# Optimization experiments

Measured on AMD Instinct MI355X. Metric: run time of the kernel, lower is better.

Reference implementation:

```python
import jax, jax.numpy as jnp
import numpy as np
from functools import partial

N_QUBITS = 8
DEPTH = 2
INPUT_DIM = 128
HIDDEN_DIM = N_QUBITS  # required: hx = o * tanh(cx) elementwise
DIM = 2 ** N_QUBITS

# Z expectation matrix: ZMAT[k, i] = +1/-1 depending on bit of basis state k at wire i
# (wire 0 is the most-significant qubit, PennyLane convention)
_bits = ((np.arange(DIM)[:, None] >> (N_QUBITS - 1 - np.arange(N_QUBITS)[None, :])) & 1)
ZMAT = jnp.asarray(1.0 - 2.0 * _bits, dtype=jnp.float32)  # [2**n, n]


def _apply_1q(state, G, wire):
    """Apply 2x2 gate G ([2,2] shared or [B,2,2] batched) on `wire`."""
    B = state.shape[0]
    left, right = 2 ** wire, 2 ** (N_QUBITS - wire - 1)
    s = state.reshape(B, left, 2, right)
    if G.ndim == 2:
        s = jnp.einsum('ij,bljr->blir', G, s)
    else:
        s = jnp.einsum('bij,bljr->blir', G, s)
    return s.reshape(B, DIM)


def _apply_cnot(state, wire):
    """CNOT with control=wire, target=wire+1 (adjacent)."""
    B = state.shape[0]
    left, right = 2 ** wire, 2 ** (N_QUBITS - wire - 2)
    s = state.reshape(B, left, 2, 2, right)
    s = jnp.concatenate([s[:, :, :1], s[:, :, 1:, ::-1]], axis=2)
    return s.reshape(B, DIM)


def quantum_gate(angles, params):
    """angles: [B, n] RX rotation angles; params: [depth, n] RY angles.
    Returns [B, n] PauliZ expectations (exact statevector simulation)."""
    B = angles.shape[0]
    state = jnp.zeros((B, DIM), dtype=jnp.complex64).at[:, 0].set(1.0)
    # RX encoding layer (batched angles)
    c = jnp.cos(angles / 2).astype(jnp.complex64)
    s = (-1j) * jnp.sin(angles / 2).astype(jnp.complex64)
    for i in range(N_QUBITS):
        G = jnp.stack([jnp.stack([c[:, i], s[:, i]], -1),
                       jnp.stack([s[:, i], c[:, i]], -1)], -2)  # [B,2,2]
        state = _apply_1q(state, G, i)
    # variational layers: RY (shared params) + CNOT chain
    cp = jnp.cos(params / 2).astype(jnp.complex64)
    sp = jnp.sin(params / 2).astype(jnp.complex64)
    for d in range(DEPTH):
        for i in range(N_QUBITS):
            G = jnp.array([[1.0, 0.0], [0.0, 1.0]], jnp.complex64)
            G = jnp.stack([jnp.stack([cp[d, i], -sp[d, i]]),
                           jnp.stack([sp[d, i], cp[d, i]])])  # [2,2]
            state = _apply_1q(state, G, i)
        for i in range(N_QUBITS - 1):
            state = _apply_cnot(state, i)
    probs = (state.real ** 2 + state.imag ** 2)  # [B, 2**n]
    return probs @ ZMAT  # [B, n]


def setup_inputs() -> dict:
    key = jax.random.key(0)
    ks = jax.random.split(key, 13)
    T, B = 256, 1024
    cat = INPUT_DIM + HIDDEN_DIM
    lin_scale = 1.0 / np.sqrt(cat)
    d = {'inputs': jax.random.normal(ks[0], (T, B, INPUT_DIM), jnp.float32)}
    for idx, g in enumerate(['f', 'i', 'g', 'o']):
        d[f'W{g}'] = jax.random.uniform(ks[1 + 3 * idx], (N_QUBITS, cat), jnp.float32, -lin_scale, lin_scale)
        d[f'b{g}'] = jax.random.uniform(ks[2 + 3 * idx], (N_QUBITS,), jnp.float32, -lin_scale, lin_scale)
        d[f'P{g}'] = jax.random.normal(ks[3 + 3 * idx], (DEPTH, N_QUBITS), jnp.float32)
    return d


def reference(inputs, Wf, bf, Pf, Wi, bi, Pi, Wg, bg, Pg, Wo, bo, Po):
    T, B, _ = inputs.shape
    h0 = jnp.zeros((B, HIDDEN_DIM), inputs.dtype)
    c0 = jnp.zeros((B, HIDDEN_DIM), inputs.dtype)

    def step(carry, x):
        hx, cx = carry
        comb = jnp.concatenate([x, hx], axis=1)  # [B, input+hidden]
        f = jax.nn.sigmoid(quantum_gate(comb @ Wf.T + bf, Pf))
        i = jax.nn.sigmoid(quantum_gate(comb @ Wi.T + bi, Pi))
        g = jnp.tanh(quantum_gate(comb @ Wg.T + bg, Pg))
        o = jax.nn.sigmoid(quantum_gate(comb @ Wo.T + bo, Po))
        cx = f * cx + i * g
        hx = o * jnp.tanh(cx)
        return (hx, cx), hx

    (hx, cx), outputs = jax.lax.scan(step, (h0, c0), inputs)
    return outputs, (hx, cx)
```

## Files before the change

### kernel.cpp

```cpp
#include <hip/hip_runtime.h>
#include <math.h>

#define TS 256
#define BB 1024
#define NQ 8
#define INDIM 128
#define CATDIM 136

typedef float v2f __attribute__((ext_vector_type(2)));

__device__ __forceinline__ float dpp_xor1(float v) {
    return __int_as_float(__builtin_amdgcn_mov_dpp(__float_as_int(v), 0xB1, 0xF, 0xF, true));
}
__device__ __forceinline__ float dpp_xor2(float v) {
    return __int_as_float(__builtin_amdgcn_mov_dpp(__float_as_int(v), 0x4E, 0xF, 0xF, true));
}
__device__ __forceinline__ float dpp_xor8(float v) {
    return __int_as_float(__builtin_amdgcn_mov_dpp(__float_as_int(v), 0x128, 0xF, 0xF, true));
}
__device__ __forceinline__ float swz_xor4(float v) {
    return __int_as_float(__builtin_amdgcn_ds_swizzle(__float_as_int(v), 0x101F));
}
__device__ __forceinline__ float swz_xor16(float v) {
    return __int_as_float(__builtin_amdgcn_ds_swizzle(__float_as_int(v), 0x401F));
}
__device__ __forceinline__ v2f mk2(float x, float y) { v2f r; r.x = x; r.y = y; return r; }
__device__ __forceinline__ v2f pk_mul(v2f a, v2f b) {
    v2f d; asm("v_pk_mul_f32 %0, %1, %2" : "=v"(d) : "v"(a), "v"(b)); return d;
}
__device__ __forceinline__ v2f pk_fma(v2f a, v2f b, v2f c) {
    v2f d; asm("v_pk_fma_f32 %0, %1, %2, %3" : "=v"(d) : "v"(a), "v"(b), "v"(c)); return d;
}

__launch_bounds__(256)
__global__ void qlstm_xproj(const float* __restrict__ x,
    const float* __restrict__ Wf, const float* __restrict__ bf,
    const float* __restrict__ Wi, const float* __restrict__ bi,
    const float* __restrict__ Wg, const float* __restrict__ bg,
    const float* __restrict__ Wo, const float* __restrict__ bo,
    float* __restrict__ xproj)
{
    const int b = blockIdx.x;
    const int wv = threadIdx.x >> 6;
    const int lane = threadIdx.x & 63;
    const int q = lane >> 3;
    const int kg = lane & 7;

    const float* Ws[4] = { Wf, Wi, Wg, Wo };
    const float* bs[4] = { bf, bi, bg, bo };
    float4 wfrag[4][4];
    float bias_w[4];
    #pragma unroll
    for (int g = 0; g < 4; ++g) {
        const float* Wq = Ws[g] + q * CATDIM + kg * 16;
        #pragma unroll
        for (int c4 = 0; c4 < 4; ++c4) wfrag[g][c4] = *(const float4*)(Wq + c4 * 4);
        bias_w[g] = bs[g][q];
    }

    float4 xv[4];
    {
        const float* xr = x + ((size_t)wv * BB + b) * INDIM + kg * 16;
        #pragma unroll
        for (int c4 = 0; c4 < 4; ++c4) xv[c4] = *(const float4*)(xr + c4 * 4);
    }

    #pragma unroll 2
    for (int i = 0; i < 64; ++i) {
        const int t = wv + i * 4;
        float4 xn[4];
        {
            int t2 = (i < 63) ? t + 4 : t;
            const float* xr = x + ((size_t)t2 * BB + b) * INDIM + kg * 16;
            #pragma unroll
            for (int c4 = 0; c4 < 4; ++c4) xn[c4] = *(const float4*)(xr + c4 * 4);
        }
        float* outrow = xproj + ((size_t)b * TS + t) * 32;
        #pragma unroll
        for (int g = 0; g < 4; ++g) {
            float p =
                xv[0].x*wfrag[g][0].x + xv[0].y*wfrag[g][0].y + xv[0].z*wfrag[g][0].z + xv[0].w*wfrag[g][0].w +
                xv[1].x*wfrag[g][1].x + xv[1].y*wfrag[g][1].y + xv[1].z*wfrag[g][1].z + xv[1].w*wfrag[g][1].w +
                xv[2].x*wfrag[g][2].x + xv[2].y*wfrag[g][2].y + xv[2].z*wfrag[g][2].z + xv[2].w*wfrag[g][2].w +
                xv[3].x*wfrag[g][3].x + xv[3].y*wfrag[g][3].y + xv[3].z*wfrag[g][3].z + xv[3].w*wfrag[g][3].w;
            p += dpp_xor1(p);
            p += dpp_xor2(p);
            p += __shfl_xor(p, 4, 64);
            if (kg == 0) outrow[g * 8 + q] = p + bias_w[g];
        }
        xv[0] = xn[0]; xv[1] = xn[1]; xv[2] = xn[2]; xv[3] = xn[3];
    }
}

__launch_bounds__(64, 1)
__global__ void qlstm_w(const float* __restrict__ xproj,
    const float* __restrict__ Wf, const float* __restrict__ Pf,
    const float* __restrict__ Wi, const float* __restrict__ Pi,
    const float* __restrict__ Wg, const float* __restrict__ Pg,
    const float* __restrict__ Wo, const float* __restrict__ Po,
    float* __restrict__ out, float* __restrict__ hst, float* __restrict__ cst)
{
    const int lane = threadIdx.x;
    const int q = lane & 7;
    const int g = (lane >> 3) & 3;
    const int el2 = lane >> 5;
    const int b = blockIdx.x * 2 + el2;

    const float* W; const float* P;
    if (g == 0)      { W = Wf; P = Pf; }
    else if (g == 1) { W = Wi; P = Pi; }
    else if (g == 2) { W = Wg; P = Pg; }
    else             { W = Wo; P = Po; }

    float Cw[8], Sw[8], hsp0[8], cp0c[8];
    #pragma unroll
    for (int w = 0; w < 8; ++w) {
        float s1, c1, s0, c0;
        __sincosf(P[8 + w], &s1, &c1);
        __sincosf(P[w], &s0, &c0);
        Cw[w] = c1; Sw[w] = s1;
        hsp0[w] = 0.5f * s0;
        cp0c[w] = c0;
    }

    v2f whp[8][4];
    #pragma unroll
    for (int j = 0; j < 8; ++j) {
        const float* Wj = W + j * CATDIM + INDIM;
        #pragma unroll
        for (int p2 = 0; p2 < 4; ++p2)
            whp[j][p2] = mk2(Wj[q ^ (2 * p2)], Wj[q ^ (2 * p2 + 1)]);
    }

    const float kk = (g == 2) ? 2.f : -1.f;
    const float Aa = (g == 2) ? 1.f : 0.f;
    const float Bb = (g == 2) ? -1.f : 1.f;

    float s0h = 0.f, s1h = 0.f, s2h = 0.f, s3h = 0.f;
    float s4h = 0.f, s5h = 0.f, s6h = 0.f, s7h = 0.f;
    float c_own = 0.f, hv = 0.f;

    const float* xbase = xproj + ((size_t)b * TS) * 32 + g * 8;
    float4 xv0 = *(const float4*)(xbase);
    float4 xv1 = *(const float4*)(xbase + 4);

    for (int t = 0; t < TS; ++t) {
        v2f hp0 = mk2(s0h, s1h), hp1 = mk2(s2h, s3h);
        v2f hp2 = mk2(s4h, s5h), hp3 = mk2(s6h, s7h);
        float xq[8] = { xv0.x, xv0.y, xv0.z, xv0.w, xv1.x, xv1.y, xv1.z, xv1.w };
        float sa[8], ca[8];
        #pragma unroll
        for (int j = 0; j < 8; ++j) {
            v2f acc = pk_mul(hp0, whp[j][0]);
            acc = pk_fma(hp1, whp[j][1], acc);
            acc = pk_fma(hp2, whp[j][2], acc);
            acc = pk_fma(hp3, whp[j][3], acc);
            float ang = xq[j] + acc.x + acc.y;
            __sincosf(ang, &sa[j], &ca[j]);
        }

        {
            int tn = (t + 1 < TS) ? t + 1 : t;
            xv0 = *(const float4*)(xbase + (size_t)tn * 32);
            xv1 = *(const float4*)(xbase + (size_t)tn * 32 + 4);
        }

        float myE = 0.f;
        float d0, d1, zr, zi;
        {
            float AmB = cp0c[0] * ca[0];
            float A_ = 0.5f + 0.5f * AmB;
            d0 = Cw[0] * A_;
            d1 = -Cw[0] * (1.f - A_);
            zr = -Sw[0] * (hsp0[0] * ca[0]);
            zi = -Sw[0] * (-0.5f * sa[0]);
        }
        #pragma unroll
        for (int w = 1; w < 8; ++w) {
            float gr = hsp0[w] * ca[w];
            float gi = -0.5f * sa[w];
            float AmB = cp0c[w] * ca[w];
            float sum = d0 + d1, dif = d0 - d1;
            float p = gr * zr, qv = gi * zi;
            float Ew = fmaf(4.f, p, sum);
            if (q == w - 1) myE = Ew;
            float u  = fmaf(AmB, dif, sum);
            float u2 = fmaf(-AmB, dif, sum);
            float t0 = fmaf(2.f, p - qv, 0.5f * u);
            float t1 = fmaf(2.f, p + qv, 0.5f * u2);
            float nzr = -Sw[w] * fmaf(gr, sum, zr);
            float nzi = -Sw[w] * fmaf(AmB, zi, gi * dif);
            d0 = Cw[w] * t0;
            d1 = -Cw[w] * t1;
            zr = nzr; zi = nzi;
        }
        if (q == 7) myE = (d0 + d1) + 2.f * zr;

        float y = __expf(kk * myE);
        float a = fmaf(Aa, y, Bb) / (y + 1.f);

        float a8 = dpp_xor8(a);
        float pAx = (g & 1) ? a8 : a;
        float pAy = (g & 1) ? a : a8;
        float pBx = swz_xor16(pAx);
        float pBy = swz_xor16(pAy);
        bool glo = (g & 2) == 0;
        float fv = glo ? pAx : pBx;
        float iv = glo ? pAy : pBy;
        float gv = glo ? pBx : pAx;
        float ov = glo ? pBy : pAy;

        c_own = fmaf(fv, c_own, iv * gv);
        float e2 = __expf(2.f * c_own);
        hv = ov * ((e2 - 1.f) / (e2 + 1.f));

        if ((lane & 24) == 0)
            out[((size_t)t * BB + b) * NQ + q] = hv;

        s0h = hv;
        s1h = dpp_xor1(s0h);
        s2h = dpp_xor2(s0h);
        s3h = dpp_xor2(s1h);
        s4h = swz_xor4(s0h);
        s5h = swz_xor4(s1h);
        s6h = swz_xor4(s2h);
        s7h = swz_xor4(s3h);
    }

    if ((lane & 24) == 0) {
        hst[b * NQ + q] = hv;
        cst[b * NQ + q] = c_own;
    }
}

extern "C" void kernel_launch(void* const* d_in, const int* in_sizes, int n_in,
                              void* d_out, int out_size, void* d_ws, size_t ws_size,
                              hipStream_t stream) {
    const float* x  = (const float*)d_in[0];
    const float* Wf = (const float*)d_in[1];
    const float* bf = (const float*)d_in[2];
    const float* Pf = (const float*)d_in[3];
    const float* Wi = (const float*)d_in[4];
    const float* bi = (const float*)d_in[5];
    const float* Pi = (const float*)d_in[6];
    const float* Wg = (const float*)d_in[7];
    const float* bg = (const float*)d_in[8];
    const float* Pg = (const float*)d_in[9];
    const float* Wo = (const float*)d_in[10];
    const float* bo = (const float*)d_in[11];
    const float* Po = (const float*)d_in[12];

    float* out = (float*)d_out;
    float* hst = out + (size_t)TS * BB * NQ;
    float* cst = hst + (size_t)BB * NQ;
    float* xproj = (float*)d_ws;

    qlstm_xproj<<<BB, 256, 0, stream>>>(x, Wf, bf, Wi, bi, Wg, bg, Wo, bo, xproj);
    qlstm_w<<<BB / 2, 64, 0, stream>>>(xproj, Wf, Pf, Wi, Pi, Wg, Pg, Wo, Po,
                                       out, hst, cst);
}
```

Measured before the change: 242.8 us.

## Use raw hardware transcendentals, prescale angles, and remap lanes for DPP-only exchanges

Pre-scales the W and bias projections by 1/(2π) so the recurrent loop can call v_sin/v_cos directly, and swaps __expf and division for v_exp with a log2e factor and v_rcp. The lane-to-(qubit, gate) mapping is changed so the hidden-state broadcast uses DPP row exchanges instead of ds_swizzle, and the gate gather uses three swizzles. The x projection is folded into the packed FMA, and the per-qubit expectation select becomes a branch-free FMA with a precomputed selector. Together these shorten the serial per-timestep dependency chain, in exchange for less accurate raw hardware sin/cos/exp/rcp with no range reduction.

```diff
diff --git a/kernel.cpp b/kernel.cpp
--- a/kernel.cpp
+++ b/kernel.cpp
@@ -6,6 +6,8 @@
 #define NQ 8
 #define INDIM 128
 #define CATDIM 136
+#define INV2PI 0.15915494309189535f
+#define LOG2E  1.4426950408889634f
 
 typedef float v2f __attribute__((ext_vector_type(2)));
 
@@ -18,12 +20,19 @@
 __device__ __forceinline__ float dpp_xor8(float v) {
     return __int_as_float(__builtin_amdgcn_mov_dpp(__float_as_int(v), 0x128, 0xF, 0xF, true));
 }
-__device__ __forceinline__ float swz_xor4(float v) {
+__device__ __forceinline__ float swz4(float v)  {
     return __int_as_float(__builtin_amdgcn_ds_swizzle(__float_as_int(v), 0x101F));
 }
-__device__ __forceinline__ float swz_xor16(float v) {
+__device__ __forceinline__ float swz16(float v) {
     return __int_as_float(__builtin_amdgcn_ds_swizzle(__float_as_int(v), 0x401F));
 }
+__device__ __forceinline__ float swz20(float v) {
+    return __int_as_float(__builtin_amdgcn_ds_swizzle(__float_as_int(v), 0x501F));
+}
+__device__ __forceinline__ float hw_sin(float x) { float r; asm("v_sin_f32 %0, %1" : "=v"(r) : "v"(x)); return r; }
+__device__ __forceinline__ float hw_cos(float x) { float r; asm("v_cos_f32 %0, %1" : "=v"(r) : "v"(x)); return r; }
+__device__ __forceinline__ float hw_exp(float x) { float r; asm("v_exp_f32 %0, %1" : "=v"(r) : "v"(x)); return r; }
+__device__ __forceinline__ float hw_rcp(float x) { float r; asm("v_rcp_f32 %0, %1" : "=v"(r) : "v"(x)); return r; }
 __device__ __forceinline__ v2f mk2(float x, float y) { v2f r; r.x = x; r.y = y; return r; }
 __device__ __forceinline__ v2f pk_mul(v2f a, v2f b) {
     v2f d; asm("v_pk_mul_f32 %0, %1, %2" : "=v"(d) : "v"(a), "v"(b)); return d;
@@ -54,8 +63,12 @@
     for (int g = 0; g < 4; ++g) {
         const float* Wq = Ws[g] + q * CATDIM + kg * 16;
         #pragma unroll
-        for (int c4 = 0; c4 < 4; ++c4) wfrag[g][c4] = *(const float4*)(Wq + c4 * 4);
-        bias_w[g] = bs[g][q];
+        for (int c4 = 0; c4 < 4; ++c4) {
+            float4 v = *(const float4*)(Wq + c4 * 4);
+            v.x *= INV2PI; v.y *= INV2PI; v.z *= INV2PI; v.w *= INV2PI;
+            wfrag[g][c4] = v;
+        }
+        bias_w[g] = bs[g][q] * INV2PI;
     }
 
     float4 xv[4];
@@ -93,7 +106,7 @@
 }
 
 __launch_bounds__(64, 1)
-__global__ void qlstm_w(const float* __restrict__ xproj,
+__global__ void qlstm_v(const float* __restrict__ xproj,
     const float* __restrict__ Wf, const float* __restrict__ Pf,
     const float* __restrict__ Wi, const float* __restrict__ Pi,
     const float* __restrict__ Wg, const float* __restrict__ Pg,
@@ -101,8 +114,8 @@
     float* __restrict__ out, float* __restrict__ hst, float* __restrict__ cst)
 {
     const int lane = threadIdx.x;
-    const int q = lane & 7;
-    const int g = (lane >> 3) & 3;
+    const int q = (lane & 1) | (lane & 2) | ((lane >> 1) & 4);
+    const int g = ((lane >> 2) & 1) | ((lane >> 3) & 2);
     const int el2 = lane >> 5;
     const int b = blockIdx.x * 2 + el2;
 
@@ -112,13 +125,14 @@
     else if (g == 2) { W = Wg; P = Pg; }
     else             { W = Wo; P = Po; }
 
-    float Cw[8], Sw[8], hsp0[8], cp0c[8];
+    float Chw[8], nSw[8], hsp0[8], cp0c[8];
     #pragma unroll
     for (int w = 0; w < 8; ++w) {
         float s1, c1, s0, c0;
         __sincosf(P[8 + w], &s1, &c1);
         __sincosf(P[w], &s0, &c0);
-        Cw[w] = c1; Sw[w] = s1;
+        Chw[w] = 0.5f * c1;
+        nSw[w] = -s1;
         hsp0[w] = 0.5f * s0;
         cp0c[w] = c0;
     }
@@ -129,12 +143,16 @@
         const float* Wj = W + j * CATDIM + INDIM;
         #pragma unroll
         for (int p2 = 0; p2 < 4; ++p2)
-            whp[j][p2] = mk2(Wj[q ^ (2 * p2)], Wj[q ^ (2 * p2 + 1)]);
+            whp[j][p2] = mk2(INV2PI * Wj[q ^ (2 * p2)], INV2PI * Wj[q ^ (2 * p2 + 1)]);
     }
 
     const float kk = (g == 2) ? 2.f : -1.f;
+    const float kl = kk * LOG2E;
     const float Aa = (g == 2) ? 1.f : 0.f;
     const float Bb = (g == 2) ? -1.f : 1.f;
+    float sel[8];
+    #pragma unroll
+    for (int i = 0; i < 8; ++i) sel[i] = (q == i) ? kl : 0.f;
 
     float s0h = 0.f, s1h = 0.f, s2h = 0.f, s3h = 0.f;
     float s4h = 0.f, s5h = 0.f, s6h = 0.f, s7h = 0.f;
@@ -151,12 +169,13 @@
         float sa[8], ca[8];
         #pragma unroll
         for (int j = 0; j < 8; ++j) {
-            v2f acc = pk_mul(hp0, whp[j][0]);
+            v2f acc = pk_fma(hp0, whp[j][0], mk2(xq[j], 0.f));
             acc = pk_fma(hp1, whp[j][1], acc);
             acc = pk_fma(hp2, whp[j][2], acc);
             acc = pk_fma(hp3, whp[j][3], acc);
-            float ang = xq[j] + acc.x + acc.y;
-            __sincosf(ang, &sa[j], &ca[j]);
+            float ang = acc.x + acc.y;
+            sa[j] = hw_sin(ang);
+            ca[j] = hw_cos(ang);
         }
 
         {
@@ -165,15 +184,16 @@
             xv1 = *(const float4*)(xbase + (size_t)tn * 32 + 4);
         }
 
-        float myE = 0.f;
+        float kE = 0.f;
         float d0, d1, zr, zi;
         {
             float AmB = cp0c[0] * ca[0];
-            float A_ = 0.5f + 0.5f * AmB;
-            d0 = Cw[0] * A_;
-            d1 = -Cw[0] * (1.f - A_);
-            zr = -Sw[0] * (hsp0[0] * ca[0]);
-            zi = -Sw[0] * (-0.5f * sa[0]);
+            float gr = hsp0[0] * ca[0];
+            float gi = -0.5f * sa[0];
+            d0 = Chw[0] * (1.f + AmB);
+            d1 = -(Chw[0] * (1.f - AmB));
+            zr = nSw[0] * gr;
+            zi = nSw[0] * gi;
         }
         #pragma unroll
         for (int w = 1; w < 8; ++w) {
@@ -183,51 +203,60 @@
             float sum = d0 + d1, dif = d0 - d1;
             float p = gr * zr, qv = gi * zi;
             float Ew = fmaf(4.f, p, sum);
-            if (q == w - 1) myE = Ew;
-            float u  = fmaf(AmB, dif, sum);
-            float u2 = fmaf(-AmB, dif, sum);
-            float t0 = fmaf(2.f, p - qv, 0.5f * u);
-            float t1 = fmaf(2.f, p + qv, 0.5f * u2);
-            float nzr = -Sw[w] * fmaf(gr, sum, zr);
-            float nzi = -Sw[w] * fmaf(AmB, zi, gi * dif);
-            d0 = Cw[w] * t0;
-            d1 = -Cw[w] * t1;
-            zr = nzr; zi = nzi;
-        }
-        if (q == 7) myE = (d0 + d1) + 2.f * zr;
-
-        float y = __expf(kk * myE);
-        float a = fmaf(Aa, y, Bb) / (y + 1.f);
-
-        float a8 = dpp_xor8(a);
-        float pAx = (g & 1) ? a8 : a;
-        float pAy = (g & 1) ? a : a8;
-        float pBx = swz_xor16(pAx);
-        float pBy = swz_xor16(pAy);
-        bool glo = (g & 2) == 0;
-        float fv = glo ? pAx : pBx;
-        float iv = glo ? pAy : pBy;
-        float gv = glo ? pBx : pAx;
-        float ov = glo ? pBy : pAy;
+            kE = fmaf(sel[w - 1], Ew, kE);
+            float ad = AmB * dif;
+            float e1 = sum + ad, e3 = sum - ad;
+            float e2 = p - qv, e4 = p + qv;
+            float T0 = fmaf(4.f, e2, e1);
+            float T1 = fmaf(4.f, e4, e3);
+            float f1 = fmaf(gr, sum, zr);
+            float f2 = gi * dif;
+            float f3 = fmaf(AmB, zi, f2);
+            d0 = Chw[w] * T0;
+            d1 = -(Chw[w] * T1);
+            zr = nSw[w] * f1;
+            zi = nSw[w] * f3;
+        }
+        {
+            float E7 = (d0 + d1) + 2.f * zr;
+            kE = fmaf(sel[7], E7, kE);
+        }
+
+        float y = hw_exp(kE);
+        float a = fmaf(Aa, y, Bb) * hw_rcp(y + 1.f);
+
+        float b4 = swz4(a);
+        float b16 = swz16(a);
+        float b20 = swz20(a);
+        bool g1b = (g & 2) != 0;
+        bool g0b = (g & 1) != 0;
+        float e0 = g1b ? b16 : a;
+        float e1s = g1b ? b20 : b4;
+        float e2s = g1b ? a : b16;
+        float e3s = g1b ? b4 : b20;
+        float fv = g0b ? e1s : e0;
+        float iv = g0b ? e0 : e1s;
+        float gv = g0b ? e3s : e2s;
+        float ov = g0b ? e2s : e3s;
 
         c_own = fmaf(fv, c_own, iv * gv);
-        float e2 = __expf(2.f * c_own);
-        hv = ov * ((e2 - 1.f) / (e2 + 1.f));
-
-        if ((lane & 24) == 0)
+        float e2c = hw_exp(c_own * (2.f * LOG2E));
+        hv = ov * ((e2c - 1.f) * hw_rcp(e2c + 1.f));
+
+        if ((lane & 0x14) == 0)
             out[((size_t)t * BB + b) * NQ + q] = hv;
 
         s0h = hv;
         s1h = dpp_xor1(s0h);
         s2h = dpp_xor2(s0h);
         s3h = dpp_xor2(s1h);
-        s4h = swz_xor4(s0h);
-        s5h = swz_xor4(s1h);
-        s6h = swz_xor4(s2h);
-        s7h = swz_xor4(s3h);
-    }
-
-    if ((lane & 24) == 0) {
+        s4h = dpp_xor8(s0h);
+        s5h = dpp_xor8(s1h);
+        s6h = dpp_xor8(s2h);
+        s7h = dpp_xor8(s3h);
+    }
+
+    if ((lane & 0x14) == 0) {
         hst[b * NQ + q] = hv;
         cst[b * NQ + q] = c_own;
     }
@@ -256,6 +285,6 @@
     float* xproj = (float*)d_ws;
 
     qlstm_xproj<<<BB, 256, 0, stream>>>(x, Wf, bf, Wi, bi, Wg, bg, Wo, bo, xproj);
-    qlstm_w<<<BB / 2, 64, 0, stream>>>(xproj, Wf, Pf, Wi, Pi, Wg, Pg, Wo, Po,
+    qlstm_v<<<BB / 2, 64, 0, stream>>>(xproj, Wf, Pf, Wi, Pi, Wg, Pg, Wo, Po,
                                        out, hst, cst);
 }
```

New measurement: 238.3 us. About the same (-1.9%).
